# Kernel optimization log

Hardware: AMD Instinct MI355X
Metric: run time of the kernel (lower is better)

## Reference

```python
import jax, jax.numpy as jnp
import numpy as np

B, S, T, H, E, K = 32, 256, 256, 4096, 64, 4
GAMMA_ROUTING = 0.5   # gamma_routing init kwarg
TEMPERATURE = 1.0     # routing temperature
EPS = 1e-6


def setup_inputs() -> dict:
    key = jax.random.key(0)
    k1, k2, k3, k4, k5 = jax.random.split(key, 5)
    input_embeds = jax.random.normal(k1, (B, S, H), dtype=jnp.float32)
    prompt_base = 0.02 * jax.random.normal(k2, (T, H), dtype=jnp.float32)
    # module inits delta to zeros; use small noise so routing blend is non-trivial
    prompt_delta = 0.01 * jax.random.normal(k3, (T, H), dtype=jnp.float32)
    LiMEs = 1.0 + jax.random.uniform(k4, (E, H), dtype=jnp.float32, minval=-0.1, maxval=0.1)
    LiME_shared = 0.1 * jax.random.normal(k5, (H,), dtype=jnp.float32)
    gamma = jnp.zeros((1,), dtype=jnp.float32)
    W_proj = jnp.eye(H, dtype=jnp.float32)  # nn.init.eye_ on input_proj.weight
    return {"input_embeds": input_embeds, "prompt_base": prompt_base,
            "prompt_delta": prompt_delta, "LiMEs": LiMEs,
            "LiME_shared": LiME_shared, "gamma": gamma, "W_proj": W_proj}


def reference(input_embeds, prompt_base, prompt_delta, LiMEs, LiME_shared, gamma, W_proj):
    # --- input conditioning (mode='mean' with projection) ---
    cond = jnp.einsum('bsh,oh->bo', input_embeds, W_proj) / input_embeds.shape[1]  # (B,H)
    hidden = prompt_base[None, :, :] + cond[:, None, :]                            # (B,T,H)
    # --- fused routing softmax over first E channels ---
    H_slice = hidden[..., :E]                        # (B,T,E)
    d_slice = prompt_delta[None, :, :E]              # (1,T,E)
    H_scale = jnp.maximum(jnp.max(jnp.abs(H_slice)), EPS)
    d_scale = jnp.maximum(jnp.max(jnp.abs(d_slice)), EPS)
    logits = ((1.0 - GAMMA_ROUTING) * (H_slice / H_scale)
              + GAMMA_ROUTING * (d_slice / d_scale)) / TEMPERATURE
    probs = jax.nn.softmax(logits, axis=-1)          # (B,T,E)
    # --- sparse top-k routing + gather-combine of LiME vectors ---
    topk_vals, topk_idx = jax.lax.top_k(probs, K)    # (B,T,K)
    topk_vals = topk_vals / jnp.maximum(topk_vals.sum(-1, keepdims=True), 1e-9)
    selected = LiMEs[topk_idx]                       # (B,T,K,H) gather
    p_mix = jnp.einsum('btk,btkh->bth', topk_vals, selected)  # (B,T,H)
    # --- blend with shared LiME and apply multiplicative prompt scale ---
    g = jax.nn.sigmoid(gamma)                        # (1,)
    scale = (1.0 - g) * p_mix + g * LiME_shared      # (B,T,H)
    prompt = (prompt_base + prompt_delta)[None, :, :] * scale
    return prompt
```

## Files before the change

### kernel.cpp

```cpp
#include <hip/hip_runtime.h>

#define BB 32
#define SS 256
#define TT 256
#define HH 4096
#define EE 64

typedef unsigned int u32;
typedef float f4 __attribute__((ext_vector_type(4)));

__global__ __launch_bounds__(256, 4) void k1_cond(const float* __restrict__ x,
                                                  const float* __restrict__ W,
                                                  float* __restrict__ cond) {
    __shared__ float X[1024];
    int id = blockIdx.x;
    int hc = id & 3;
    int sc = (id >> 2) & 7;
    int b  = id >> 5;
    int h0 = threadIdx.x * 4;
    int hb = hc * 1024;
    const float* src = x + ((size_t)b * SS + sc * 32) * HH + hb + h0;
    f4 acc = 0.f;
#pragma unroll 8
    for (int s = 0; s < 32; ++s) {
        f4 v = __builtin_nontemporal_load((const f4*)(src + (size_t)s * HH));
        acc += v;
    }
    *(f4*)(X + h0) = acc;
    __syncthreads();
    int wave = threadIdx.x >> 6, lane = threadIdx.x & 63;
    for (int e = wave; e < EE; e += 4) {
        const float* wrow = W + (size_t)e * HH + hb;
        float s = 0.f;
#pragma unroll
        for (int i = 0; i < 4; ++i) {
            int h = i * 256 + lane * 4;
            f4 wv = *(const f4*)(wrow + h);
            f4 xv = *(const f4*)(X + h);
            f4 p = wv * xv;
            s += p.x + p.y + p.z + p.w;
        }
#pragma unroll
        for (int off = 32; off; off >>= 1) s += __shfl_xor(s, off);
        if (lane == 0) atomicAdd(cond + b * EE + e, s * (1.0f / SS));
    }
}

__global__ __launch_bounds__(256) void k3_scales(const float* __restrict__ pb,
                                                 const float* __restrict__ pd,
                                                 const float* __restrict__ cond,
                                                 u32* __restrict__ scaleBits) {
    int tid = blockIdx.x * 256 + threadIdx.x;
    float hmax = 0.f, dmax = 0.f;
    for (int idx = tid; idx < BB * TT * EE; idx += 32768) {
        int e = idx & 63, t = (idx >> 6) & 255, b = idx >> 14;
        float v = pb[t * HH + e] + cond[b * EE + e];
        hmax = fmaxf(hmax, fabsf(v));
    }
    for (int idx = tid; idx < TT * EE; idx += 32768) {
        int e = idx & 63, t = idx >> 6;
        dmax = fmaxf(dmax, fabsf(pd[t * HH + e]));
    }
#pragma unroll
    for (int off = 32; off; off >>= 1) {
        hmax = fmaxf(hmax, __shfl_xor(hmax, off));
        dmax = fmaxf(dmax, __shfl_xor(dmax, off));
    }
    __shared__ float sh[4], sd[4];
    int wave = threadIdx.x >> 6, lane = threadIdx.x & 63;
    if (lane == 0) { sh[wave] = hmax; sd[wave] = dmax; }
    __syncthreads();
    if (threadIdx.x == 0) {
        float h = sh[0], d = sd[0];
#pragma unroll
        for (int i = 1; i < 4; ++i) { h = fmaxf(h, sh[i]); d = fmaxf(d, sd[i]); }
        atomicMax(scaleBits + 0, __float_as_uint(h));
        atomicMax(scaleBits + 1, __float_as_uint(d));
    }
}

__global__ __launch_bounds__(256, 4) void k4_main(const float* __restrict__ pb,
                                                  const float* __restrict__ pd,
                                                  const float* __restrict__ limes,
                                                  const float* __restrict__ shr,
                                                  const float* __restrict__ gamma,
                                                  const float* __restrict__ cond,
                                                  const u32* __restrict__ scaleBits,
                                                  float* __restrict__ out) {
    __shared__ float Pbd[HH];
    __shared__ float Gs[HH];
    int t  = blockIdx.x >> 3;
    int bq = blockIdx.x & 7;
    float g = 1.f / (1.f + __expf(-gamma[0]));
    size_t rb = (size_t)t * HH;

    {
        const f4* Pb = (const f4*)(pb + rb);
        const f4* Pd = (const f4*)(pd + rb);
        const f4* Sh = (const f4*)shr;
#pragma unroll
        for (int i = 0; i < 4; ++i) {
            int j = i * 256 + threadIdx.x;
            f4 a = Pb[j];
            f4 c = Pd[j];
            f4 s = Sh[j];
            ((f4*)Pbd)[j] = a + c;
            ((f4*)Gs)[j]  = g * s;
        }
    }
    __syncthreads();

    int wave = threadIdx.x >> 6, lane = threadIdx.x & 63;
    int b = bq * 4 + wave;

    float Hs = fmaxf(__uint_as_float(scaleBits[0]), 1e-6f);
    float Ds = fmaxf(__uint_as_float(scaleBits[1]), 1e-6f);

    float logit = 0.5f * (pb[rb + lane] + cond[b * EE + lane]) / Hs
                + 0.5f * pd[rb + lane] / Ds;

    int selIdx[4]; float selL[4];
    float work = logit;
#pragma unroll
    for (int k = 0; k < 4; ++k) {
        float v = work; int vi = lane;
#pragma unroll
        for (int off = 32; off; off >>= 1) {
            float ov = __shfl_xor(v, off);
            int   oi = __shfl_xor(vi, off);
            if (ov > v || (ov == v && oi < vi)) { v = ov; vi = oi; }
        }
        selIdx[k] = vi; selL[k] = v;
        if (lane == vi) work = -1e30f;
    }
    float m = selL[0];
    float w0 = __expf(selL[0] - m), w1 = __expf(selL[1] - m);
    float w2 = __expf(selL[2] - m), w3 = __expf(selL[3] - m);
    float inv = 1.f / (w0 + w1 + w2 + w3);
    float om = 1.f - g;
    float c0 = w0 * inv * om, c1 = w1 * inv * om;
    float c2 = w2 * inv * om, c3 = w3 * inv * om;

    const float* L0 = limes + (size_t)selIdx[0] * HH;
    const float* L1 = limes + (size_t)selIdx[1] * HH;
    const float* L2 = limes + (size_t)selIdx[2] * HH;
    const float* L3 = limes + (size_t)selIdx[3] * HH;
    size_t ob = ((size_t)b * TT + t) * HH;

#pragma unroll
    for (int i = 0; i < 16; ++i) {
        int h = i * 256 + lane * 4;
        f4 fp = *(const f4*)(Pbd + h);
        f4 fg = *(const f4*)(Gs + h);
        f4 f0 = *(const f4*)(L0 + h);
        f4 f1 = *(const f4*)(L1 + h);
        f4 f2 = *(const f4*)(L2 + h);
        f4 f3 = *(const f4*)(L3 + h);
        f4 mix = fg + c0 * f0 + c1 * f1 + c2 * f2 + c3 * f3;
        f4 r = fp * mix;
        __builtin_nontemporal_store(r, (f4*)(out + ob + h));
    }
}

extern "C" void kernel_launch(void* const* d_in, const int* in_sizes, int n_in,
                              void* d_out, int out_size, void* d_ws, size_t ws_size,
                              hipStream_t stream) {
    const float *x = 0, *pb = 0, *pd = 0, *limes = 0, *shr = 0, *gm = 0, *W = 0;
    for (int i = 0; i < n_in; ++i) {
        const float* p = (const float*)d_in[i];
        switch (in_sizes[i]) {
            case BB * SS * HH: x = p; break;
            case TT * HH: if (!pb) pb = p; else pd = p; break;
            case EE * HH: limes = p; break;
            case HH: shr = p; break;
            case 1: gm = p; break;
            case HH * HH: W = p; break;
        }
    }
    float* out = (float*)d_out;

    u32* scaleBits = (u32*)d_ws;
    float* cond = (float*)d_ws + 2;

    hipMemsetAsync(d_ws, 0, (2 + BB * EE) * sizeof(float), stream);
    k1_cond<<<BB * 8 * 4, 256, 0, stream>>>(x, W, cond);
    k3_scales<<<128, 256, 0, stream>>>(pb, pd, cond, scaleBits);
    k4_main<<<BB * TT / 4, 256, 0, stream>>>(pb, pd, limes, shr, gm, cond,
                                             scaleBits, out);
}
```

Baseline: 310.1 us.

## Assign one output row per block in main kernel, drop LDS staging

The main kernel now gives each (b,t) row its own 256-thread block instead of one wave per row with four rows per block. The LDS staging of prompt_base+delta and the scaled shared LiME, along with the block barrier, is gone; those values are re-read from global/L2 per row. Expert indices are made wave-uniform with readfirstlane so expert row loads can use scalar addressing, and the scale-reduction kernel gets four times more blocks. All four waves in a block redundantly recompute the routing top-k, and the shared operands are reloaded once per row instead of once per four rows.

```diff
diff --git a/kernel.cpp b/kernel.cpp
--- a/kernel.cpp
+++ b/kernel.cpp
@@ -52,12 +52,12 @@
                                                  u32* __restrict__ scaleBits) {
     int tid = blockIdx.x * 256 + threadIdx.x;
     float hmax = 0.f, dmax = 0.f;
-    for (int idx = tid; idx < BB * TT * EE; idx += 32768) {
+    for (int idx = tid; idx < BB * TT * EE; idx += 131072) {
         int e = idx & 63, t = (idx >> 6) & 255, b = idx >> 14;
         float v = pb[t * HH + e] + cond[b * EE + e];
         hmax = fmaxf(hmax, fabsf(v));
     }
-    for (int idx = tid; idx < TT * EE; idx += 32768) {
+    for (int idx = tid; idx < TT * EE; idx += 131072) {
         int e = idx & 63, t = idx >> 6;
         dmax = fmaxf(dmax, fabsf(pd[t * HH + e]));
     }
@@ -87,35 +87,15 @@
                                                   const float* __restrict__ cond,
                                                   const u32* __restrict__ scaleBits,
                                                   float* __restrict__ out) {
-    __shared__ float Pbd[HH];
-    __shared__ float Gs[HH];
-    int t  = blockIdx.x >> 3;
-    int bq = blockIdx.x & 7;
-    float g = 1.f / (1.f + __expf(-gamma[0]));
-    size_t rb = (size_t)t * HH;
-
-    {
-        const f4* Pb = (const f4*)(pb + rb);
-        const f4* Pd = (const f4*)(pd + rb);
-        const f4* Sh = (const f4*)shr;
-#pragma unroll
-        for (int i = 0; i < 4; ++i) {
-            int j = i * 256 + threadIdx.x;
-            f4 a = Pb[j];
-            f4 c = Pd[j];
-            f4 s = Sh[j];
-            ((f4*)Pbd)[j] = a + c;
-            ((f4*)Gs)[j]  = g * s;
-        }
-    }
-    __syncthreads();
-
-    int wave = threadIdx.x >> 6, lane = threadIdx.x & 63;
-    int b = bq * 4 + wave;
+    int row = blockIdx.x;
+    int t = row >> 5, b = row & 31;
+    int lane = threadIdx.x & 63;
 
     float Hs = fmaxf(__uint_as_float(scaleBits[0]), 1e-6f);
     float Ds = fmaxf(__uint_as_float(scaleBits[1]), 1e-6f);
+    float g = 1.f / (1.f + __expf(-gamma[0]));
 
+    size_t rb = (size_t)t * HH;
     float logit = 0.5f * (pb[rb + lane] + cond[b * EE + lane]) / Hs
                 + 0.5f * pd[rb + lane] / Ds;
 
@@ -141,24 +121,27 @@
     float c0 = w0 * inv * om, c1 = w1 * inv * om;
     float c2 = w2 * inv * om, c3 = w3 * inv * om;
 
-    const float* L0 = limes + (size_t)selIdx[0] * HH;
-    const float* L1 = limes + (size_t)selIdx[1] * HH;
-    const float* L2 = limes + (size_t)selIdx[2] * HH;
-    const float* L3 = limes + (size_t)selIdx[3] * HH;
-    size_t ob = ((size_t)b * TT + t) * HH;
+    const float* L0 = limes + (size_t)__builtin_amdgcn_readfirstlane(selIdx[0]) * HH;
+    const float* L1 = limes + (size_t)__builtin_amdgcn_readfirstlane(selIdx[1]) * HH;
+    const float* L2 = limes + (size_t)__builtin_amdgcn_readfirstlane(selIdx[2]) * HH;
+    const float* L3 = limes + (size_t)__builtin_amdgcn_readfirstlane(selIdx[3]) * HH;
+    const float* Pb = pb + rb;
+    const float* Pd = pd + rb;
+    float* O = out + ((size_t)b * TT + t) * HH;
 
 #pragma unroll
-    for (int i = 0; i < 16; ++i) {
-        int h = i * 256 + lane * 4;
-        f4 fp = *(const f4*)(Pbd + h);
-        f4 fg = *(const f4*)(Gs + h);
+    for (int c = 0; c < 4; ++c) {
+        int h = c * 1024 + threadIdx.x * 4;
+        f4 fb = *(const f4*)(Pb + h);
+        f4 fd = *(const f4*)(Pd + h);
+        f4 fs = *(const f4*)(shr + h);
         f4 f0 = *(const f4*)(L0 + h);
         f4 f1 = *(const f4*)(L1 + h);
         f4 f2 = *(const f4*)(L2 + h);
         f4 f3 = *(const f4*)(L3 + h);
-        f4 mix = fg + c0 * f0 + c1 * f1 + c2 * f2 + c3 * f3;
-        f4 r = fp * mix;
-        __builtin_nontemporal_store(r, (f4*)(out + ob + h));
+        f4 mix = g * fs + c0 * f0 + c1 * f1 + c2 * f2 + c3 * f3;
+        f4 r = (fb + fd) * mix;
+        __builtin_nontemporal_store(r, (f4*)(O + h));
     }
 }
 
@@ -184,7 +167,7 @@
 
     hipMemsetAsync(d_ws, 0, (2 + BB * EE) * sizeof(float), stream);
     k1_cond<<<BB * 8 * 4, 256, 0, stream>>>(x, W, cond);
-    k3_scales<<<128, 256, 0, stream>>>(pb, pd, cond, scaleBits);
-    k4_main<<<BB * TT / 4, 256, 0, stream>>>(pb, pd, limes, shr, gm, cond,
-                                             scaleBits, out);
+    k3_scales<<<512, 256, 0, stream>>>(pb, pd, cond, scaleBits);
+    k4_main<<<BB * TT, 256, 0, stream>>>(pb, pd, limes, shr, gm, cond,
+                                         scaleBits, out);
 }
```

Result: slower. 341.1 us (+10.0%).
